# Performance work log

Measured on AMD Instinct MI355X. Metric: run time of the kernel, lower is better.

## Reference

```python
import jax, jax.numpy as jnp
import numpy as np

V = 30000   # vocab (len(en_dict))
D = 256     # embed/d_model
H = 4       # heads
DK = D // H
N = 1024    # max_len
B = 16      # batch
HID = 256   # ffn hidden
NEG = -1e10
SCALE = 1.0 / np.sqrt(DK)


def setup_inputs() -> dict:
    key = jax.random.key(0)
    ks = jax.random.split(key, 24)
    g = lambda i, shape, s=0.02: jax.random.normal(ks[i], shape, jnp.float32) * s
    return {
        'input_ids': jax.random.randint(ks[0], (B, N), 0, V),
        'attention_mask': jnp.ones((B, N), jnp.int32),
        'emb_W': g(1, (D, V)), 'emb_b': g(2, (D,)),
        'wq': g(3, (D, D)), 'bq': g(4, (D,)),
        'wk': g(5, (D, D)), 'bk': g(6, (D,)),
        'wv': g(7, (D, D)), 'bv': g(8, (D,)),
        'fc_w': g(9, (D, D)), 'fc_b': g(10, (D,)),
        'ff_w1': g(11, (HID, D)), 'ff_b1': g(12, (HID,)),
        'ff_w2': g(13, (D, HID)), 'ff_b2': g(14, (D,)),
        'h1_w': g(15, (128, D)), 'h1_b': g(16, (128,)),
        'bn_gamma': jnp.ones((128,)), 'bn_beta': jnp.zeros((128,)),
        'bn_mean': jnp.zeros((128,)), 'bn_var': jnp.ones((128,)),
        'h2_w': g(17, (1, 128)), 'h2_b': g(18, (1,)),
    }


def _pos_encoding():
    pos = jnp.arange(N, dtype=jnp.float32)[:, None]
    down = jnp.exp(jnp.arange(0, D, 2, dtype=jnp.float32) * (-np.log(10000.0) / D))
    ang = pos * down  # (N, D/2)
    pe = jnp.zeros((N, D), jnp.float32)
    pe = pe.at[:, 0::2].set(jnp.sin(ang) / 10.0)
    pe = pe.at[:, 1::2].set(jnp.cos(ang) / 10.0)
    return pe


def _forward(input_ids, attention_mask, emb_W, emb_b, wq, bq, wk, bk, wv, bv,
             fc_w, fc_b, ff_w1, ff_b1, ff_w2, ff_b2, h1_w, h1_b,
             bn_gamma, bn_beta, bn_mean, bn_var, h2_w, h2_b):
    # one-hot @ W^T + b  ==  direct column gather of W
    x = emb_W.T[input_ids] + emb_b          # (B, N, D)
    x = x + _pos_encoding()                  # dropout off (eval)

    # --- multi-head self-attention with per-sample span mask ---
    def heads(w, b):
        return (jnp.einsum('bnd,ed->bne', x, w) + b).reshape(B, N, H, DK).transpose(0, 2, 1, 3)
    q, k, v = heads(wq, bq), heads(wk, bk), heads(wv, bv)
    scores = jnp.einsum('bhnd,bhmd->bhnm', q, k) * SCALE  # (B,H,N,N)

    m = attention_mask.astype(bool)
    start = jnp.argmax(m, axis=1)                    # first True
    end = N - 1 - jnp.argmax(m[:, ::-1], axis=1)     # last True (exclusive end in slice)
    idx = jnp.arange(N)
    in_span = (idx[None, :] >= start[:, None]) & (idx[None, :] < end[:, None])  # (B,N)
    allowed = in_span[:, :, None] & in_span[:, None, :]                         # (B,N,N)
    scores = scores + jnp.where(allowed, 0.0, NEG)[:, None, :, :]

    p = jax.nn.softmax(scores, axis=-1)
    att = jnp.einsum('bhnm,bhmd->bhnd', p, v).transpose(0, 2, 1, 3).reshape(B, N, D)
    att = jnp.einsum('bnd,ed->bne', att, fc_w) + fc_b
    x = x + att

    # --- feed-forward (replaces x, no residual; dropout off; exact GELU) ---
    h = jax.nn.gelu(jnp.einsum('bnd,hd->bnh', x, ff_w1) + ff_b1, approximate=False)
    x = jnp.einsum('bnh,dh->bnd', h, ff_w2) + ff_b2

    # --- mean pool + MLP head (BatchNorm in eval mode) ---
    pooled = jnp.mean(x, axis=1)                      # (B, D)
    h = pooled @ h1_w.T + h1_b                        # (B, 128)
    h = (h - bn_mean) / jnp.sqrt(bn_var + 1e-5) * bn_gamma + bn_beta
    h = jax.nn.relu(h)
    return h @ h2_w.T + h2_b                          # (B, 1)


def reference(input_ids, attention_mask, emb_W, emb_b, wq, bq, wk, bk, wv, bv,
              fc_w, fc_b, ff_w1, ff_b1, ff_w2, ff_b2, h1_w, h1_b,
              bn_gamma, bn_beta, bn_mean, bn_var, h2_w, h2_b):
    return _forward(input_ids, attention_mask, emb_W, emb_b, wq, bq, wk, bk, wv, bv,
                    fc_w, fc_b, ff_w1, ff_b1, ff_w2, ff_b2, h1_w, h1_b,
                    bn_gamma, bn_beta, bn_mean, bn_var, h2_w, h2_b)
```

## Files before the change

### kernel.cpp

```cpp
#include <hip/hip_runtime.h>
#include <math.h>

#define VOCAB 30000
#define DMODEL 256
#define NHEAD 4
#define SEQ 1024
#define BATCH 16
#define MROWS (BATCH*SEQ)
#define SL2 0.18033688011112042f
#define NEG2 (-1.4426950408889634e10f)

typedef __attribute__((ext_vector_type(8))) short bf16x8;
typedef __attribute__((ext_vector_type(4))) float f32x4;

#if __has_builtin(__builtin_amdgcn_exp2f)
#define EXP2F __builtin_amdgcn_exp2f
#else
#define EXP2F exp2f
#endif

__device__ __forceinline__ unsigned short f2b(float f) {
    unsigned int u = __float_as_uint(f);
    unsigned int r = (u + 0x7FFFu + ((u >> 16) & 1u)) >> 16;
    return (unsigned short)r;
}
__device__ __forceinline__ unsigned short f2b_trunc(float f) {
    return (unsigned short)(__float_as_uint(f) >> 16);
}
__device__ __forceinline__ float b2f(unsigned short s) {
    unsigned int u = ((unsigned int)s) << 16;
    return __uint_as_float(u);
}

__global__ __launch_bounds__(256) void prep_kernel(const int* __restrict__ mask, int* __restrict__ spans,
                                                   float* __restrict__ pe,
                                                   const float* __restrict__ wq, const float* __restrict__ wk,
                                                   const float* __restrict__ wv, const float* __restrict__ bq,
                                                   const float* __restrict__ bk, const float* __restrict__ bv,
                                                   unsigned short* __restrict__ wqkv, float* __restrict__ bias768,
                                                   const float* __restrict__ fcw, const float* __restrict__ f1w,
                                                   const float* __restrict__ f2w, unsigned short* __restrict__ wb3,
                                                   const float* __restrict__ embW, const float* __restrict__ eb,
                                                   unsigned short* __restrict__ embT) {
    int blk = blockIdx.x;
    int t = threadIdx.x;
    if (blk < 64) {
        __shared__ double down[128];
        if (t < 128) down[t] = exp((double)(2 * t) * (-9.210340371976184 / 256.0));
        __syncthreads();
        int d2 = t & 127, half = t >> 7;
        #pragma unroll
        for (int i = 0; i < 8; i++) {
            int n = blk * 16 + half * 8 + i;
            double ang = (double)n * down[d2];
            pe[n * DMODEL + 2 * d2]     = (float)(sin(ang) * 0.1);
            pe[n * DMODEL + 2 * d2 + 1] = (float)(cos(ang) * 0.1);
        }
    } else if (blk < 80) {
        int b = blk - 64;
        __shared__ int smin, smax;
        if (t == 0) { smin = SEQ; smax = -1; }
        __syncthreads();
        int lmin = SEQ, lmax = -1;
        for (int i = t; i < SEQ; i += 256) {
            if (mask[b * SEQ + i] != 0) { lmin = min(lmin, i); lmax = max(lmax, i); }
        }
        atomicMin(&smin, lmin);
        atomicMax(&smax, lmax);
        __syncthreads();
        if (t == 0) {
            int st, en;
            if (smax < 0) { st = 0; en = SEQ - 1; }
            else          { st = smin; en = smax; }
            spans[b * 2] = st; spans[b * 2 + 1] = en;
        }
    } else if (blk < 849) {
        int cb = blk - 80;
        if (cb < 768) {
            const float* src = (cb < 256) ? wq : (cb < 512) ? wk : wv;
            wqkv[cb * 256 + t] = f2b(src[(cb & 255) * 256 + t]);
        } else {
            for (int j = t; j < 768; j += 256)
                bias768[j] = (j < 256) ? bq[j] : (j < 512) ? bk[j - 256] : bv[j - 512];
        }
    } else if (blk < 1617) {
        int cb = blk - 849;
        const float* src = (cb < 256) ? fcw : (cb < 512) ? f1w : f2w;
        wb3[cb * 256 + t] = f2b(src[(cb & 255) * 256 + t]);
    } else {
        __shared__ float tsh[32][33];
        int tb = blk - 1617;
        int bx = tb % 938, by = tb / 938;
        int tx = t & 31, ty = t >> 5;
        int c0 = bx * 32, r0 = by * 32;
        for (int i = 0; i < 32; i += 8) {
            int r = r0 + ty + i, c = c0 + tx;
            if (c < VOCAB) tsh[ty + i][tx] = embW[(size_t)r * VOCAB + c];
        }
        __syncthreads();
        float ebv = eb[r0 + tx];
        for (int i = 0; i < 32; i += 8) {
            int c = c0 + ty + i, r = r0 + tx;
            if (c < VOCAB) embT[(size_t)c * DMODEL + r] = f2b(tsh[tx][ty + i] + ebv);
        }
    }
}

__global__ __launch_bounds__(512) void qkv_kernel(const int* __restrict__ ids,
                                                  const unsigned short* __restrict__ embT,
                                                  const float* __restrict__ pe,
                                                  const unsigned short* __restrict__ W,
                                                  const float* __restrict__ bias,
                                                  unsigned short* __restrict__ x0b,
                                                  unsigned short* __restrict__ Qb,
                                                  unsigned short* __restrict__ Kb,
                                                  unsigned short* __restrict__ Vt) {
    __shared__ unsigned short XA[4 * 64 * 64];
    __shared__ unsigned short Bs[2][256 * 64];
    int tid = threadIdx.x;
    int m0 = blockIdx.x * 64;
    int w = tid >> 6, l = tid & 63;
    int wrow = w >> 1, wcol = w & 1;
    int lg = l >> 4, ll = l & 15;
    int bb = m0 >> 10;

    #pragma unroll
    for (int i = 0; i < 4; i++) {
        int s = tid + i * 512;
        int row = s >> 5;
        int kb = (s & 31) * 16;
        int kt = kb >> 7, within = kb & 127;
        int swz = within ^ ((row & 7) << 4);
        int tok = m0 + row;
        int id = ids[tok];
        int n = tok & (SEQ - 1);
        bf16x8 ev = *(const bf16x8*)((const char*)embT + (size_t)id * 512 + kb);
        float4 p0 = *(const float4*)((const char*)pe + (size_t)n * 1024 + kb * 2);
        float4 p1 = *(const float4*)((const char*)pe + (size_t)n * 1024 + kb * 2 + 16);
        bf16x8 xv;
        xv[0] = (short)f2b(b2f((unsigned short)ev[0]) + p0.x);
        xv[1] = (short)f2b(b2f((unsigned short)ev[1]) + p0.y);
        xv[2] = (short)f2b(b2f((unsigned short)ev[2]) + p0.z);
        xv[3] = (short)f2b(b2f((unsigned short)ev[3]) + p0.w);
        xv[4] = (short)f2b(b2f((unsigned short)ev[4]) + p1.x);
        xv[5] = (short)f2b(b2f((unsigned short)ev[5]) + p1.y);
        xv[6] = (short)f2b(b2f((unsigned short)ev[6]) + p1.z);
        xv[7] = (short)f2b(b2f((unsigned short)ev[7]) + p1.w);
        *(bf16x8*)((char*)XA + kt * 8192 + row * 128 + swz) = xv;
        *(bf16x8*)((char*)x0b + (size_t)tok * 512 + kb) = xv;
    }

    for (int nb = 0; nb < 3; nb++) {
        f32x4 acc[8] = {};
        #pragma unroll
        for (int i = 0; i < 4; i++) {
            int s = tid + i * 512;
            int row = s >> 3, kb = (s & 7) * 16;
            int swz = kb ^ ((row & 7) << 4);
            float4 bv = *(const float4*)((const char*)W + (size_t)(nb * 256 + row) * 512 + kb);
            *(float4*)((char*)Bs[0] + row * 128 + swz) = bv;
        }
        __syncthreads();

        for (int kt = 0; kt < 4; kt++) {
            int cur = kt & 1;
            float4 pre[4];
            if (kt < 3) {
                #pragma unroll
                for (int i = 0; i < 4; i++) {
                    int s = tid + i * 512;
                    int row = s >> 3, kb = (s & 7) * 16;
                    pre[i] = *(const float4*)((const char*)W + (size_t)(nb * 256 + row) * 512 + (kt + 1) * 128 + kb);
                }
            }
            int arow = wrow * 16 + ll;
            bf16x8 af[2];
            #pragma unroll
            for (int ks = 0; ks < 2; ks++)
                af[ks] = *(const bf16x8*)((const char*)XA + kt * 8192 + arow * 128 + ((lg * 16 + ks * 64) ^ ((arow & 7) << 4)));
            #pragma unroll
            for (int nf = 0; nf < 8; nf++) {
                int brow = wcol * 128 + nf * 16 + ll;
                #pragma unroll
                for (int ks = 0; ks < 2; ks++) {
                    bf16x8 bf = *(const bf16x8*)((const char*)Bs[cur] + brow * 128 + ((lg * 16 + ks * 64) ^ ((brow & 7) << 4)));
                    acc[nf] = __builtin_amdgcn_mfma_f32_16x16x32_bf16(af[ks], bf, acc[nf], 0, 0, 0);
                }
            }
            if (kt < 3) {
                #pragma unroll
                for (int i = 0; i < 4; i++) {
                    int s = tid + i * 512;
                    int row = s >> 3, kb = (s & 7) * 16;
                    int swz = kb ^ ((row & 7) << 4);
                    *(float4*)((char*)Bs[cur ^ 1] + row * 128 + swz) = pre[i];
                }
            }
            __syncthreads();
        }
        #pragma unroll
        for (int nf = 0; nf < 8; nf++) {
            int col = wcol * 128 + nf * 16 + ll;
            float bv = bias[nb * 256 + col];
            int hh = col >> 6, dk = col & 63;
            if (nb == 2) {
                unsigned int lo = (unsigned int)f2b(acc[nf][0] + bv) | ((unsigned int)f2b(acc[nf][1] + bv) << 16);
                unsigned int hi = (unsigned int)f2b(acc[nf][2] + bv) | ((unsigned int)f2b(acc[nf][3] + bv) << 16);
                int ns = (m0 & 1023) + wrow * 16 + lg * 4;
                unsigned int* dst = (unsigned int*)(Vt + ((((size_t)bb * 4 + hh) * 64) + dk) * 1024 + ns);
                dst[0] = lo;
                dst[1] = hi;
            } else {
                #pragma unroll
                for (int r2 = 0; r2 < 4; r2++) {
                    int ns = (m0 & 1023) + wrow * 16 + lg * 4 + r2;
                    float v = acc[nf][r2] + bv;
                    if (nb == 0)
                        Qb[((((size_t)bb * 4 + hh) * 1024) + ns) * 64 + dk] = f2b(v * SL2);
                    else
                        Kb[((((size_t)bb * 4 + hh) * 1024) + ns) * 64 + dk] = f2b(v);
                }
            }
        }
    }
}

__global__ __launch_bounds__(512) void attn_coop(const unsigned short* __restrict__ Qb,
                                                 const unsigned short* __restrict__ Kb,
                                                 const unsigned short* __restrict__ Vt,
                                                 const int* __restrict__ spans,
                                                 unsigned short* __restrict__ attb) {
    __shared__ unsigned short Ks[2][64 * 64];
    __shared__ unsigned short Vs[2][64 * 64];
    __shared__ __align__(16) unsigned short Ps[8][16 * 72];
    int tid = threadIdx.x;
    int w = tid >> 6, l = tid & 63;
    int id = blockIdx.x;
    int c = id & 7, rest = id >> 3;
    int bh = c * 8 + (rest >> 3);
    int qg = rest & 7;
    int q0 = qg * 128 + w * 16;
    int b = bh >> 2, h = bh & 3;
    int lg = l >> 4, ll = l & 15;
    const char* Kp = (const char*)(Kb + (size_t)bh * SEQ * 64);
    const char* Vp = (const char*)(Vt + (size_t)bh * 64 * SEQ);
    const unsigned short* Qp = Qb + (size_t)bh * SEQ * 64;
    int start = spans[b * 2], end = spans[b * 2 + 1];

    bf16x8 qf[2];
    #pragma unroll
    for (int ks = 0; ks < 2; ks++)
        qf[ks] = *(const bf16x8*)(Qp + (size_t)(q0 + ll) * 64 + lg * 8 + ks * 32);

    bf16x8 ones;
    #pragma unroll
    for (int i = 0; i < 8; i++) ones[i] = (short)0x3F80;

    f32x4 o[4] = {};
    f32x4 accl = {};
    bool rowok[4];
    #pragma unroll
    for (int r2 = 0; r2 < 4; r2++) {
        int rr = q0 + lg * 4 + r2;
        rowok[r2] = (rr >= start) && (rr < end);
    }

    int srow = tid >> 3, skb = (tid & 7) * 16;
    int sswz = skb ^ ((srow & 7) << 4);

    {
        float4 kv0v = *(const float4*)(Kp + (size_t)srow * 128 + skb);
        float4 vv0 = *(const float4*)(Vp + (size_t)srow * 2048 + skb);
        *(float4*)((char*)Ks[0] + srow * 128 + sswz) = kv0v;
        *(float4*)((char*)Vs[0] + srow * 128 + sswz) = vv0;
    }

    for (int ct = 0; ct < 16; ct++) {
        int cur = ct & 1;
        int kv0 = ct * 64;
        __syncthreads();

        float4 kreg, vreg;
        if (ct < 15) {
            int kvn = kv0 + 64;
            kreg = *(const float4*)(Kp + (size_t)(kvn + srow) * 128 + skb);
            vreg = *(const float4*)(Vp + (size_t)srow * 2048 + kvn * 2 + skb);
        }

        f32x4 s4[4];
        #pragma unroll
        for (int nf = 0; nf < 4; nf++) {
            int cc = kv0 + nf * 16 + ll;
            float ci = ((cc >= start) && (cc < end)) ? 0.f : NEG2;
            f32x4 cv = { ci, ci, ci, ci };
            s4[nf] = cv;
        }
        #pragma unroll
        for (int ks = 0; ks < 2; ks++)
            #pragma unroll
            for (int nf = 0; nf < 4; nf++) {
                int row = nf * 16 + ll;
                bf16x8 kf = *(const bf16x8*)((const char*)Ks[cur] + row * 128 + ((lg * 16 + ks * 64) ^ ((row & 7) << 4)));
                s4[nf] = __builtin_amdgcn_mfma_f32_16x16x32_bf16(qf[ks], kf, s4[nf], 0, 0, 0);
            }

        #pragma unroll
        for (int nf = 0; nf < 4; nf++)
            #pragma unroll
            for (int r2 = 0; r2 < 4; r2++) {
                float sv = rowok[r2] ? s4[nf][r2] : 0.f;
                s4[nf][r2] = EXP2F(sv);
            }

        #pragma unroll
        for (int nf = 0; nf < 4; nf++)
            #pragma unroll
            for (int r2 = 0; r2 < 4; r2++)
                Ps[w][(lg * 4 + r2) * 72 + nf * 16 + ll] = f2b_trunc(s4[nf][r2]);

        bf16x8 pa[2];
        #pragma unroll
        for (int ks = 0; ks < 2; ks++)
            pa[ks] = *(const bf16x8*)(&Ps[w][ll * 72 + lg * 8 + ks * 32]);

        #pragma unroll
        for (int ks = 0; ks < 2; ks++)
            #pragma unroll
            for (int cf = 0; cf < 4; cf++) {
                int row = cf * 16 + ll;
                bf16x8 vf = *(const bf16x8*)((const char*)Vs[cur] + row * 128 + ((lg * 16 + ks * 64) ^ ((row & 7) << 4)));
                o[cf] = __builtin_amdgcn_mfma_f32_16x16x32_bf16(pa[ks], vf, o[cf], 0, 0, 0);
            }
        #pragma unroll
        for (int ks = 0; ks < 2; ks++)
            accl = __builtin_amdgcn_mfma_f32_16x16x32_bf16(pa[ks], ones, accl, 0, 0, 0);

        if (ct < 15) {
            *(float4*)((char*)Ks[cur ^ 1] + srow * 128 + sswz) = kreg;
            *(float4*)((char*)Vs[cur ^ 1] + srow * 128 + sswz) = vreg;
        }
    }

    #pragma unroll
    for (int r2 = 0; r2 < 4; r2++) {
        float inv = 1.f / accl[r2];
        int row = q0 + lg * 4 + r2;
        #pragma unroll
        for (int cf = 0; cf < 4; cf++) {
            int dk = cf * 16 + ll;
            attb[((size_t)b * SEQ + row) * 256 + h * 64 + dk] = f2b(o[cf][r2] * inv);
        }
    }
}

__global__ __launch_bounds__(512) void ffn_kernel(const unsigned short* __restrict__ attb,
                                                  const unsigned short* __restrict__ x0b,
                                                  const unsigned short* __restrict__ W3,
                                                  const float* __restrict__ fcb,
                                                  const float* __restrict__ f1b,
                                                  const float* __restrict__ f2bv,
                                                  float* __restrict__ part) {
    __shared__ unsigned short BufA[4 * 64 * 64];
    __shared__ unsigned short BufB[4 * 64 * 64];
    __shared__ unsigned short Bs[2][256 * 64];
    int tid = threadIdx.x;
    int m0 = blockIdx.x * 64;
    int w = tid >> 6, l = tid & 63;
    int wrow = w >> 1, wcol = w & 1;
    int lg = l >> 4, ll = l & 15;
    int arow = wrow * 16 + ll;

    #pragma unroll
    for (int i = 0; i < 4; i++) {
        int s = tid + i * 512;
        int row = s >> 5;
        int kb = (s & 31) * 16;
        int kt = kb >> 7, within = kb & 127;
        int swz = within ^ ((row & 7) << 4);
        float4 av = *(const float4*)((const char*)attb + (size_t)(m0 + row) * 512 + kb);
        *(float4*)((char*)BufA + kt * 8192 + row * 128 + swz) = av;
    }

    #pragma unroll
    for (int phase = 0; phase < 3; phase++) {
        const unsigned short* Wp = W3 + phase * 65536;
        const char* Asrc = (phase == 1) ? (const char*)BufB : (const char*)BufA;
        f32x4 acc[8] = {};
        #pragma unroll
        for (int i = 0; i < 4; i++) {
            int s = tid + i * 512;
            int row = s >> 3, kb = (s & 7) * 16;
            int swz = kb ^ ((row & 7) << 4);
            float4 bv = *(const float4*)((const char*)Wp + (size_t)row * 512 + kb);
            *(float4*)((char*)Bs[0] + row * 128 + swz) = bv;
        }
        __syncthreads();

        for (int kt = 0; kt < 4; kt++) {
            int cur = kt & 1;
            float4 pre[4];
            if (kt < 3) {
                #pragma unroll
                for (int i = 0; i < 4; i++) {
                    int s = tid + i * 512;
                    int row = s >> 3, kb = (s & 7) * 16;
                    pre[i] = *(const float4*)((const char*)Wp + (size_t)row * 512 + (kt + 1) * 128 + kb);
                }
            }
            bf16x8 af[2];
            #pragma unroll
            for (int ks = 0; ks < 2; ks++)
                af[ks] = *(const bf16x8*)(Asrc + kt * 8192 + arow * 128 + ((lg * 16 + ks * 64) ^ ((arow & 7) << 4)));
            #pragma unroll
            for (int nf = 0; nf < 8; nf++) {
                int brow = wcol * 128 + nf * 16 + ll;
                #pragma unroll
                for (int ks = 0; ks < 2; ks++) {
                    bf16x8 bf = *(const bf16x8*)((const char*)Bs[cur] + brow * 128 + ((lg * 16 + ks * 64) ^ ((brow & 7) << 4)));
                    acc[nf] = __builtin_amdgcn_mfma_f32_16x16x32_bf16(af[ks], bf, acc[nf], 0, 0, 0);
                }
            }
            if (kt < 3) {
                #pragma unroll
                for (int i = 0; i < 4; i++) {
                    int s = tid + i * 512;
                    int row = s >> 3, kb = (s & 7) * 16;
                    int swz = kb ^ ((row & 7) << 4);
                    *(float4*)((char*)Bs[cur ^ 1] + row * 128 + swz) = pre[i];
                }
            }
            __syncthreads();
        }

        if (phase == 0) {
            #pragma unroll
            for (int nf = 0; nf < 8; nf++) {
                int col = wcol * 128 + nf * 16 + ll;
                float bv = fcb[col];
                int kt = col >> 6;
                int byteoff = (2 * (col & 63));
                #pragma unroll
                for (int r2 = 0; r2 < 4; r2++) {
                    int row = wrow * 16 + lg * 4 + r2;
                    *(unsigned short*)((char*)BufB + kt * 8192 + row * 128 + (byteoff ^ ((row & 7) << 4))) = f2b(acc[nf][r2] + bv);
                }
            }
            __syncthreads();
            #pragma unroll
            for (int i = 0; i < 4; i++) {
                int s = tid + i * 512;
                int row = s >> 5;
                int kb = (s & 31) * 16;
                int kt = kb >> 7, within = kb & 127;
                int swz = within ^ ((row & 7) << 4);
                bf16x8* dst = (bf16x8*)((char*)BufB + kt * 8192 + row * 128 + swz);
                bf16x8 xv = *dst;
                bf16x8 rv = *(const bf16x8*)((const char*)x0b + (size_t)(m0 + row) * 512 + kb);
                bf16x8 res;
                #pragma unroll
                for (int jj = 0; jj < 8; jj++)
                    res[jj] = (short)f2b(b2f((unsigned short)xv[jj]) + b2f((unsigned short)rv[jj]));
                *dst = res;
            }
        } else if (phase == 1) {
            #pragma unroll
            for (int nf = 0; nf < 8; nf++) {
                int col = wcol * 128 + nf * 16 + ll;
                float bv = f1b[col];
                int kt = col >> 6;
                int byteoff = (2 * (col & 63));
                #pragma unroll
                for (int r2 = 0; r2 < 4; r2++) {
                    int row = wrow * 16 + lg * 4 + r2;
                    float v = acc[nf][r2] + bv;
                    v = 0.5f * v * (1.f + erff(v * 0.70710678118654752f));
                    *(unsigned short*)((char*)BufA + kt * 8192 + row * 128 + (byteoff ^ ((row & 7) << 4))) = f2b(v);
                }
            }
        } else {
            int bb = m0 >> 10;
            int chunk = ((m0 & 1023) >> 4) + wrow;
            #pragma unroll
            for (int nf = 0; nf < 8; nf++) {
                int col = wcol * 128 + nf * 16 + ll;
                float s_ = acc[nf][0] + acc[nf][1] + acc[nf][2] + acc[nf][3];
                s_ += __shfl_xor(s_, 16);
                s_ += __shfl_xor(s_, 32);
                s_ += 16.f * f2bv[col];
                if (lg == 0)
                    part[((size_t)bb * 64 + chunk) * 256 + col] = s_;
            }
        }
    }
}

__global__ __launch_bounds__(128) void head2_kernel(const float* __restrict__ part,
                                                    const float* __restrict__ h1_w, const float* __restrict__ h1_b,
                                                    const float* __restrict__ g, const float* __restrict__ be,
                                                    const float* __restrict__ mu, const float* __restrict__ var,
                                                    const float* __restrict__ h2_w, const float* __restrict__ h2_b,
                                                    float* __restrict__ out) {
    int b = blockIdx.x, j = threadIdx.x;
    __shared__ float pl[256];
    __shared__ float red[128];
    float s0 = 0.f, s1 = 0.f;
    for (int ch = 0; ch < 64; ch++) {
        s0 += part[((size_t)b * 64 + ch) * 256 + j];
        s1 += part[((size_t)b * 64 + ch) * 256 + j + 128];
    }
    pl[j] = s0 * (1.f / 1024.f);
    pl[j + 128] = s1 * (1.f / 1024.f);
    __syncthreads();
    float s = 0.f;
    for (int d = 0; d < 256; d++) s = fmaf(pl[d], h1_w[j * 256 + d], s);
    s += h1_b[j];
    s = (s - mu[j]) / sqrtf(var[j] + 1e-5f) * g[j] + be[j];
    s = fmaxf(s, 0.f);
    red[j] = s * h2_w[j];
    __syncthreads();
    for (int off = 64; off; off >>= 1) {
        if (j < off) red[j] += red[j + off];
        __syncthreads();
    }
    if (j == 0) out[b] = red[0] + h2_b[0];
}

extern "C" void kernel_launch(void* const* d_in, const int* in_sizes, int n_in,
                              void* d_out, int out_size, void* d_ws, size_t ws_size,
                              hipStream_t stream) {
    (void)in_sizes; (void)n_in; (void)out_size; (void)ws_size;
    const int*   ids    = (const int*)d_in[0];
    const int*   amask  = (const int*)d_in[1];
    const float* emb_W  = (const float*)d_in[2];
    const float* emb_b  = (const float*)d_in[3];
    const float* wq = (const float*)d_in[4],  *bq = (const float*)d_in[5];
    const float* wk = (const float*)d_in[6],  *bk = (const float*)d_in[7];
    const float* wv = (const float*)d_in[8],  *bv = (const float*)d_in[9];
    const float* fcw = (const float*)d_in[10], *fcb = (const float*)d_in[11];
    const float* f1w = (const float*)d_in[12], *f1b = (const float*)d_in[13];
    const float* f2w = (const float*)d_in[14], *f2b_ = (const float*)d_in[15];
    const float* h1w = (const float*)d_in[16], *h1b = (const float*)d_in[17];
    const float* bng = (const float*)d_in[18], *bnb = (const float*)d_in[19];
    const float* bnm = (const float*)d_in[20], *bnv = (const float*)d_in[21];
    const float* h2w = (const float*)d_in[22], *h2b = (const float*)d_in[23];
    float* out = (float*)d_out;
    float* ws = (float*)d_ws;

    const size_t O_PE   = 0;
    const size_t O_EMBT = O_PE + 262144;
    const size_t O_X0B  = O_EMBT + 3840000;
    const size_t O_Q    = O_X0B + 2097152;
    const size_t O_K    = O_Q + 2097152;
    const size_t O_V    = O_K + 2097152;
    const size_t O_ATT  = O_V + 2097152;
    const size_t O_WQKV = O_ATT + 2097152;
    const size_t O_WB3  = O_WQKV + 98304;
    const size_t O_B768 = O_WB3 + 98304;
    const size_t O_PART = O_B768 + 768;
    const size_t O_SPAN = O_PART + 262144;

    float* pe   = ws + O_PE;
    unsigned short* embT = (unsigned short*)(ws + O_EMBT);
    unsigned short* x0b  = (unsigned short*)(ws + O_X0B);
    unsigned short* Qb   = (unsigned short*)(ws + O_Q);
    unsigned short* Kb   = (unsigned short*)(ws + O_K);
    unsigned short* Vt   = (unsigned short*)(ws + O_V);
    unsigned short* attb = (unsigned short*)(ws + O_ATT);
    unsigned short* wqkv = (unsigned short*)(ws + O_WQKV);
    unsigned short* wb3  = (unsigned short*)(ws + O_WB3);
    float* bias768 = ws + O_B768;
    float* part = ws + O_PART;
    int* spans  = (int*)(ws + O_SPAN);

    prep_kernel<<<1617 + 938 * 8, 256, 0, stream>>>(amask, spans, pe,
                                                    wq, wk, wv, bq, bk, bv, wqkv, bias768,
                                                    fcw, f1w, f2w, wb3,
                                                    emb_W, emb_b, embT);

    qkv_kernel<<<256, 512, 0, stream>>>(ids, embT, pe, wqkv, bias768, x0b, Qb, Kb, Vt);

    attn_coop<<<512, 512, 0, stream>>>(Qb, Kb, Vt, spans, attb);

    ffn_kernel<<<256, 512, 0, stream>>>(attb, x0b, wb3, fcb, f1b, f2b_, part);

    head2_kernel<<<BATCH, 128, 0, stream>>>(part, h1w, h1b, bng, bnb, bnm, bnv, h2w, h2b, out);
}
```

Baseline: 92.61 us.

## Process two query row tiles per wave in attention to reuse K/V fragments

Each wave in the attention kernel now handles 32 query rows (two 16-row MFMA tiles) instead of 16. Every K and V fragment read from shared memory therefore feeds two MFMAs, which halves LDS traffic and global K/V staging per query row, and the grid drops from 512 to 256 blocks. A wave-uniform check also skips the per-row mask select when all of the wave's rows are inside the span. In exchange, register use and the per-wave P buffer double, and with fewer blocks the MI355X's CUs may be less fully occupied.

```diff
diff --git a/kernel.cpp b/kernel.cpp
--- a/kernel.cpp
+++ b/kernel.cpp
@@ -232,14 +232,14 @@
                                                  unsigned short* __restrict__ attb) {
     __shared__ unsigned short Ks[2][64 * 64];
     __shared__ unsigned short Vs[2][64 * 64];
-    __shared__ __align__(16) unsigned short Ps[8][16 * 72];
+    __shared__ __align__(16) unsigned short Ps[8][32 * 72];
     int tid = threadIdx.x;
     int w = tid >> 6, l = tid & 63;
     int id = blockIdx.x;
     int c = id & 7, rest = id >> 3;
-    int bh = c * 8 + (rest >> 3);
-    int qg = rest & 7;
-    int q0 = qg * 128 + w * 16;
+    int bh = c * 8 + (rest >> 2);
+    int qg = rest & 3;
+    int q0 = qg * 256 + w * 32;
     int b = bh >> 2, h = bh & 3;
     int lg = l >> 4, ll = l & 15;
     const char* Kp = (const char*)(Kb + (size_t)bh * SEQ * 64);
@@ -247,23 +247,30 @@
     const unsigned short* Qp = Qb + (size_t)bh * SEQ * 64;
     int start = spans[b * 2], end = spans[b * 2 + 1];
 
-    bf16x8 qf[2];
+    bf16x8 qf[2][2];
     #pragma unroll
-    for (int ks = 0; ks < 2; ks++)
-        qf[ks] = *(const bf16x8*)(Qp + (size_t)(q0 + ll) * 64 + lg * 8 + ks * 32);
+    for (int mf = 0; mf < 2; mf++)
+        #pragma unroll
+        for (int ks = 0; ks < 2; ks++)
+            qf[mf][ks] = *(const bf16x8*)(Qp + (size_t)(q0 + mf * 16 + ll) * 64 + lg * 8 + ks * 32);
 
     bf16x8 ones;
     #pragma unroll
     for (int i = 0; i < 8; i++) ones[i] = (short)0x3F80;
 
-    f32x4 o[4] = {};
-    f32x4 accl = {};
-    bool rowok[4];
+    f32x4 o[2][4] = {};
+    f32x4 accl[2] = {};
+    bool rowok[2][4];
+    bool aok = true;
     #pragma unroll
-    for (int r2 = 0; r2 < 4; r2++) {
-        int rr = q0 + lg * 4 + r2;
-        rowok[r2] = (rr >= start) && (rr < end);
-    }
+    for (int mf = 0; mf < 2; mf++)
+        #pragma unroll
+        for (int r2 = 0; r2 < 4; r2++) {
+            int rr = q0 + mf * 16 + lg * 4 + r2;
+            rowok[mf][r2] = (rr >= start) && (rr < end);
+            aok = aok && rowok[mf][r2];
+        }
+    bool skipmask = __all(aok ? 1 : 0);
 
     int srow = tid >> 3, skb = (tid & 7) * 16;
     int sswz = skb ^ ((srow & 7) << 4);
@@ -287,13 +294,13 @@
             vreg = *(const float4*)(Vp + (size_t)srow * 2048 + kvn * 2 + skb);
         }
 
-        f32x4 s4[4];
+        f32x4 s4[2][4];
         #pragma unroll
         for (int nf = 0; nf < 4; nf++) {
             int cc = kv0 + nf * 16 + ll;
             float ci = ((cc >= start) && (cc < end)) ? 0.f : NEG2;
             f32x4 cv = { ci, ci, ci, ci };
-            s4[nf] = cv;
+            s4[0][nf] = cv; s4[1][nf] = cv;
         }
         #pragma unroll
         for (int ks = 0; ks < 2; ks++)
@@ -301,39 +308,59 @@
             for (int nf = 0; nf < 4; nf++) {
                 int row = nf * 16 + ll;
                 bf16x8 kf = *(const bf16x8*)((const char*)Ks[cur] + row * 128 + ((lg * 16 + ks * 64) ^ ((row & 7) << 4)));
-                s4[nf] = __builtin_amdgcn_mfma_f32_16x16x32_bf16(qf[ks], kf, s4[nf], 0, 0, 0);
-            }
-
-        #pragma unroll
-        for (int nf = 0; nf < 4; nf++)
-            #pragma unroll
-            for (int r2 = 0; r2 < 4; r2++) {
-                float sv = rowok[r2] ? s4[nf][r2] : 0.f;
-                s4[nf][r2] = EXP2F(sv);
-            }
-
-        #pragma unroll
-        for (int nf = 0; nf < 4; nf++)
-            #pragma unroll
-            for (int r2 = 0; r2 < 4; r2++)
-                Ps[w][(lg * 4 + r2) * 72 + nf * 16 + ll] = f2b_trunc(s4[nf][r2]);
-
-        bf16x8 pa[2];
-        #pragma unroll
-        for (int ks = 0; ks < 2; ks++)
-            pa[ks] = *(const bf16x8*)(&Ps[w][ll * 72 + lg * 8 + ks * 32]);
-
+                #pragma unroll
+                for (int mf = 0; mf < 2; mf++)
+                    s4[mf][nf] = __builtin_amdgcn_mfma_f32_16x16x32_bf16(qf[mf][ks], kf, s4[mf][nf], 0, 0, 0);
+            }
+
+        if (!skipmask) {
+            #pragma unroll
+            for (int mf = 0; mf < 2; mf++)
+                #pragma unroll
+                for (int nf = 0; nf < 4; nf++)
+                    #pragma unroll
+                    for (int r2 = 0; r2 < 4; r2++)
+                        s4[mf][nf][r2] = rowok[mf][r2] ? s4[mf][nf][r2] : 0.f;
+        }
+        #pragma unroll
+        for (int mf = 0; mf < 2; mf++)
+            #pragma unroll
+            for (int nf = 0; nf < 4; nf++)
+                #pragma unroll
+                for (int r2 = 0; r2 < 4; r2++)
+                    s4[mf][nf][r2] = EXP2F(s4[mf][nf][r2]);
+
+        #pragma unroll
+        for (int mf = 0; mf < 2; mf++)
+            #pragma unroll
+            for (int nf = 0; nf < 4; nf++)
+                #pragma unroll
+                for (int r2 = 0; r2 < 4; r2++)
+                    Ps[w][(mf * 16 + lg * 4 + r2) * 72 + nf * 16 + ll] = f2b_trunc(s4[mf][nf][r2]);
+
+        bf16x8 pa[2][2];
+        #pragma unroll
+        for (int rf = 0; rf < 2; rf++) {
+            int row = rf * 16 + ll;
+            #pragma unroll
+            for (int ks = 0; ks < 2; ks++)
+                pa[rf][ks] = *(const bf16x8*)(&Ps[w][row * 72 + lg * 8 + ks * 32]);
+        }
         #pragma unroll
         for (int ks = 0; ks < 2; ks++)
             #pragma unroll
             for (int cf = 0; cf < 4; cf++) {
                 int row = cf * 16 + ll;
                 bf16x8 vf = *(const bf16x8*)((const char*)Vs[cur] + row * 128 + ((lg * 16 + ks * 64) ^ ((row & 7) << 4)));
-                o[cf] = __builtin_amdgcn_mfma_f32_16x16x32_bf16(pa[ks], vf, o[cf], 0, 0, 0);
+                #pragma unroll
+                for (int rf = 0; rf < 2; rf++)
+                    o[rf][cf] = __builtin_amdgcn_mfma_f32_16x16x32_bf16(pa[rf][ks], vf, o[rf][cf], 0, 0, 0);
             }
         #pragma unroll
         for (int ks = 0; ks < 2; ks++)
-            accl = __builtin_amdgcn_mfma_f32_16x16x32_bf16(pa[ks], ones, accl, 0, 0, 0);
+            #pragma unroll
+            for (int rf = 0; rf < 2; rf++)
+                accl[rf] = __builtin_amdgcn_mfma_f32_16x16x32_bf16(pa[rf][ks], ones, accl[rf], 0, 0, 0);
 
         if (ct < 15) {
             *(float4*)((char*)Ks[cur ^ 1] + srow * 128 + sswz) = kreg;
@@ -342,15 +369,17 @@
     }
 
     #pragma unroll
-    for (int r2 = 0; r2 < 4; r2++) {
-        float inv = 1.f / accl[r2];
-        int row = q0 + lg * 4 + r2;
-        #pragma unroll
-        for (int cf = 0; cf < 4; cf++) {
-            int dk = cf * 16 + ll;
-            attb[((size_t)b * SEQ + row) * 256 + h * 64 + dk] = f2b(o[cf][r2] * inv);
-        }
-    }
+    for (int rf = 0; rf < 2; rf++)
+        #pragma unroll
+        for (int r2 = 0; r2 < 4; r2++) {
+            float inv = 1.f / accl[rf][r2];
+            int row = q0 + rf * 16 + lg * 4 + r2;
+            #pragma unroll
+            for (int cf = 0; cf < 4; cf++) {
+                int dk = cf * 16 + ll;
+                attb[((size_t)b * SEQ + row) * 256 + h * 64 + dk] = f2b(o[rf][cf][r2] * inv);
+            }
+        }
 }
 
 __global__ __launch_bounds__(512) void ffn_kernel(const unsigned short* __restrict__ attb,
@@ -579,7 +608,7 @@
 
     qkv_kernel<<<256, 512, 0, stream>>>(ids, embT, pe, wqkv, bias768, x0b, Qb, Kb, Vt);
 
-    attn_coop<<<512, 512, 0, stream>>>(Qb, Kb, Vt, spans, attb);
+    attn_coop<<<256, 512, 0, stream>>>(Qb, Kb, Vt, spans, attb);
 
     ffn_kernel<<<256, 512, 0, stream>>>(attb, x0b, wb3, fcb, f1b, f2b_, part);
 
```

Result: no change. 93.50 us (+1.0%).
